# Performance work log

Measured on AMD Instinct MI355X. Metric: run time of the kernel, lower is better.

## Reference

```python
import jax, jax.numpy as jnp
import numpy as np

D_MODEL = 1024
HEADS = 16
SEQ = 2048
BATCH = 4
NEG_INF = -1e9
LN_EPS = 1e-5


def setup_inputs() -> dict:
    key = jax.random.key(0)
    ks = jax.random.split(key, 10)
    B, S, D = BATCH, SEQ, D_MODEL
    # xavier_uniform bound for square D x D linear
    bound = np.sqrt(6.0 / (D + D))
    def xavier(k):
        return jax.random.uniform(k, (D, D), jnp.float32, -bound, bound)
    return {
        "q": jax.random.normal(ks[0], (B, S, D), jnp.float32),
        "k": jax.random.normal(ks[1], (B, S, D), jnp.float32),
        "v": jax.random.normal(ks[2], (B, S, D), jnp.float32),
        "Wq": xavier(ks[3]),
        "Wk": xavier(ks[4]),
        "Wv": xavier(ks[5]),
        "Wo": xavier(ks[6]),
        "ln_gamma": jnp.ones((D,), jnp.float32),
        "ln_beta": jnp.zeros((D,), jnp.float32),
        "sen_len": jax.random.randint(ks[7], (B,), 1, S + 1, jnp.int32),
    }


def reference(q, k, v, Wq, Wk, Wv, Wo, ln_gamma, ln_beta, sen_len):
    B, S, D = q.shape
    H = HEADS
    d = D // H
    residual = q
    # projections (Linear with weight W applies x @ W.T)
    qh = jnp.einsum('bsd,ed->bse', q, Wq).reshape(B, S, H, d).transpose(0, 2, 1, 3)
    kh = jnp.einsum('bsd,ed->bse', k, Wk).reshape(B, S, H, d).transpose(0, 2, 1, 3)
    vh = jnp.einsum('bsd,ed->bse', v, Wv).reshape(B, S, H, d).transpose(0, 2, 1, 3)
    # scores [B,H,S,S]
    scores = jnp.einsum('bhqd,bhkd->bhqk', qh, kh) / np.sqrt(d).astype(np.float32)
    # padding mask on keys: j >= sen_len[b]; causal mask: j > i
    pad = jnp.arange(S)[None, :] >= sen_len[:, None]          # [B, S]
    causal = jnp.triu(jnp.ones((S, S), bool), 1)               # [S, S]
    mask = pad[:, None, None, :] | causal[None, None, :, :]
    scores = jnp.where(mask, NEG_INF, scores)
    att = jax.nn.softmax(scores, axis=-1)
    ctx = jnp.einsum('bhqk,bhkd->bhqd', att, vh)               # [B,H,S,d]
    ctx = ctx.transpose(0, 2, 1, 3).reshape(B, S, D)
    out = jnp.einsum('bsd,ed->bse', ctx, Wo)
    out = out + residual
    mean = out.mean(-1, keepdims=True)
    var = out.var(-1, keepdims=True)
    out = (out - mean) * jax.lax.rsqrt(var + LN_EPS) * ln_gamma + ln_beta
    return out
```

## Files before the change

### kernel.cpp

```cpp
#include <hip/hip_runtime.h>

typedef __bf16 bf16;
typedef bf16 bf16x8 __attribute__((ext_vector_type(8)));
typedef bf16 bf16x4 __attribute__((ext_vector_type(4)));
typedef float f32x4 __attribute__((ext_vector_type(4)));

#define ASYNC16(gp, lp) __builtin_amdgcn_global_load_lds( \
    (__attribute__((address_space(1))) void*)(const void*)(gp), \
    (__attribute__((address_space(3))) void*)(lp), 16, 0, 0)

__device__ __forceinline__ bf16x8 cvt2(const float4 a, const float4 b) {
    bf16x8 t;
    t[0] = (bf16)a.x; t[1] = (bf16)a.y; t[2] = (bf16)a.z; t[3] = (bf16)a.w;
    t[4] = (bf16)b.x; t[5] = (bf16)b.y; t[6] = (bf16)b.z; t[7] = (bf16)b.w;
    return t;
}

__global__ __launch_bounds__(256)
void cvt_w1(const float* __restrict__ W, bf16* __restrict__ out)
{
    const int i = blockIdx.x * 256 + threadIdx.x;
    const float4 a = ((const float4*)W)[i * 2];
    const float4 b = ((const float4*)W)[i * 2 + 1];
    *(bf16x8*)&out[(size_t)i * 8] = cvt2(a, b);
}

__global__ __launch_bounds__(256)
void cvt_w3(const float* __restrict__ W0, const float* __restrict__ W1,
            const float* __restrict__ W2, bf16* __restrict__ out)
{
    const int z = blockIdx.y;
    const float* src = (z == 0) ? W0 : (z == 1) ? W1 : W2;
    const int i = blockIdx.x * 256 + threadIdx.x;
    const float4 a = ((const float4*)src)[i * 2];
    const float4 b = ((const float4*)src)[i * 2 + 1];
    *(bf16x8*)&out[((size_t)z << 20) + (size_t)i * 8] = cvt2(a, b);
}

__global__ __launch_bounds__(256, 2)
void proj_gemm(const float* __restrict__ q, const float* __restrict__ k,
               const float* __restrict__ v, const bf16* __restrict__ Wb3,
               const int* __restrict__ sen_len,
               bf16* __restrict__ Qp, bf16* __restrict__ Kp, bf16* __restrict__ Vt)
{
    constexpr int K = 1024;
    __shared__ __align__(16) bf16 As[2][128 * 32];
    __shared__ __align__(16) bf16 Bs[2][128 * 32];

    const int z = blockIdx.z;
    const int flat = blockIdx.y * 8 + blockIdx.x;
    const int m0   = (flat & 63) * 128;
    const int n0   = (flat >> 6) * 128;

    if (z != 0) {
        const int s0 = m0 & 2047;
        if (s0 >= sen_len[m0 >> 11]) return;
    }

    const float* A = (z == 0) ? q : (z == 1) ? k : v;
    const bf16* W = Wb3 + ((size_t)z << 20);

    const int tid  = threadIdx.x;
    const int lane = tid & 63;
    const int w    = tid >> 6;
    const int wr   = w >> 1, wc = w & 1;

    f32x4 acc[4][4] = {};

    for (int k0 = 0; k0 < K; k0 += 64) {
        #pragma unroll
        for (int half = 0; half < 2; ++half) {
            #pragma unroll
            for (int i = 0; i < 2; ++i) {
                const int c   = w * 128 + i * 64 + lane;
                const int row = c >> 2, kg = c & 3;
                const int kb  = k0 + half * 32 + kg * 8;
                ASYNC16(W + (size_t)(n0 + row) * K + kb, &Bs[half][c * 8]);
                const float* ap = A + (size_t)(m0 + row) * K + kb;
                *(bf16x8*)&As[half][c * 8] = cvt2(*(const float4*)ap, *(const float4*)(ap + 4));
            }
        }
        __syncthreads();
        #pragma unroll
        for (int kk = 0; kk < 2; ++kk) {
            bf16x8 af[4], bfr[4];
            #pragma unroll
            for (int t = 0; t < 4; ++t) {
                af[t]  = *(const bf16x8*)&As[kk][(wr * 64 + t * 16 + (lane & 15)) * 32 + (lane >> 4) * 8];
                bfr[t] = *(const bf16x8*)&Bs[kk][(wc * 64 + t * 16 + (lane & 15)) * 32 + (lane >> 4) * 8];
            }
            #pragma unroll
            for (int mt = 0; mt < 4; ++mt)
                #pragma unroll
                for (int nt = 0; nt < 4; ++nt)
                    acc[mt][nt] = __builtin_amdgcn_mfma_f32_16x16x32_bf16(af[mt], bfr[nt], acc[mt][nt], 0, 0, 0);
        }
        __syncthreads();
    }

    #pragma unroll
    for (int mt = 0; mt < 4; ++mt) {
        #pragma unroll
        for (int nt = 0; nt < 4; ++nt) {
            const int mbase = m0 + wr * 64 + mt * 16 + ((lane >> 4) << 2);
            const int n     = n0 + wc * 64 + nt * 16 + (lane & 15);
            if (z < 2) {
                bf16* out = (z == 0) ? Qp : Kp;
                #pragma unroll
                for (int r = 0; r < 4; ++r)
                    out[(size_t)(mbase + r) * 1024 + n] = (bf16)acc[mt][nt][r];
            } else {
                const int h = n >> 6, dd = n & 63;
                const int b = mbase >> 11, s = mbase & 2047;
                bf16x4 v4;
                #pragma unroll
                for (int r = 0; r < 4; ++r) v4[r] = (bf16)acc[mt][nt][r];
                *(bf16x4*)&Vt[(((size_t)(b * 16 + h)) * 64 + dd) * 2048 + s] = v4;
            }
        }
    }
}

__global__ __launch_bounds__(256, 2)
void gemm_out(const bf16* __restrict__ A, const bf16* __restrict__ W,
              const float* __restrict__ R, float* __restrict__ out)
{
    constexpr int K = 1024;
    __shared__ __align__(16) bf16 As[2][128 * 32];
    __shared__ __align__(16) bf16 Bs[2][128 * 32];

    const int tid  = threadIdx.x;
    const int lane = tid & 63;
    const int w    = tid >> 6;
    const int wr   = w >> 1, wc = w & 1;
    const int flat = blockIdx.y * 8 + blockIdx.x;
    const int m0   = (flat & 63) * 128;
    const int n0   = (flat >> 6) * 128;

    f32x4 acc[4][4] = {};

    for (int k0 = 0; k0 < K; k0 += 64) {
        #pragma unroll
        for (int half = 0; half < 2; ++half) {
            #pragma unroll
            for (int i = 0; i < 2; ++i) {
                const int c   = w * 128 + i * 64 + lane;
                const int row = c >> 2, kg = c & 3;
                const int kb  = k0 + half * 32 + kg * 8;
                ASYNC16(A + (size_t)(m0 + row) * K + kb, &As[half][c * 8]);
                ASYNC16(W + (size_t)(n0 + row) * K + kb, &Bs[half][c * 8]);
            }
        }
        __syncthreads();
        #pragma unroll
        for (int kk = 0; kk < 2; ++kk) {
            bf16x8 af[4], bfr[4];
            #pragma unroll
            for (int t = 0; t < 4; ++t) {
                af[t]  = *(const bf16x8*)&As[kk][(wr * 64 + t * 16 + (lane & 15)) * 32 + (lane >> 4) * 8];
                bfr[t] = *(const bf16x8*)&Bs[kk][(wc * 64 + t * 16 + (lane & 15)) * 32 + (lane >> 4) * 8];
            }
            #pragma unroll
            for (int mt = 0; mt < 4; ++mt)
                #pragma unroll
                for (int nt = 0; nt < 4; ++nt)
                    acc[mt][nt] = __builtin_amdgcn_mfma_f32_16x16x32_bf16(af[mt], bfr[nt], acc[mt][nt], 0, 0, 0);
        }
        __syncthreads();
    }

    #pragma unroll
    for (int mt = 0; mt < 4; ++mt) {
        #pragma unroll
        for (int nt = 0; nt < 4; ++nt) {
            const int mbase = m0 + wr * 64 + mt * 16 + ((lane >> 4) << 2);
            const int n     = n0 + wc * 64 + nt * 16 + (lane & 15);
            #pragma unroll
            for (int r = 0; r < 4; ++r) {
                const size_t idx = (size_t)(mbase + r) * 1024 + n;
                out[idx] = acc[mt][nt][r] + R[idx];
            }
        }
    }
}

__global__ __launch_bounds__(256, 2)
void attn_kernel(const bf16* __restrict__ Qp, const bf16* __restrict__ Kp,
                 const bf16* __restrict__ Vt, const int* __restrict__ sen_len,
                 bf16* __restrict__ ctx)
{
    const int qt = gridDim.x - 1 - blockIdx.x;
    const int h = blockIdx.y, b = blockIdx.z;
    const int q0 = qt * 128;
    const int slen = sen_len[b];
    const int tid = threadIdx.x, lane = tid & 63, w = tid >> 6;
    const int wr = w >> 1, wc = w & 1;
    const float SCALE = 0.125f;
    const float SHIFT = 20.0f;

    __shared__ __align__(16) bf16 Ps[128 * 136];
    __shared__ float psum[2][128];

    bf16x8 qf[4][2];
    const bf16* Qbase = Qp + ((size_t)(b * 2048 + q0)) * 1024 + h * 64;
    #pragma unroll
    for (int mt = 0; mt < 4; ++mt)
        #pragma unroll
        for (int kk = 0; kk < 2; ++kk)
            qf[mt][kk] = *(const bf16x8*)(Qbase + (size_t)(wr * 64 + mt * 16 + (lane & 15)) * 1024
                                          + kk * 32 + (lane >> 4) * 8);

    f32x4 o[4][2] = {};
    float lsum[4][4] = {};

    const int jlim = min(q0 + 128, slen);
    const int nkt  = (jlim + 127) >> 7;

    const bf16* Kbh = Kp + (size_t)b * 2048 * 1024 + h * 64;
    const bf16* Vbh = Vt + (size_t)(b * 16 + h) * 64 * 2048;

    for (int kt = 0; kt < nkt; ++kt) {
        const int k0 = kt * 128;

        f32x4 sf[4][4] = {};
        #pragma unroll
        for (int kk = 0; kk < 2; ++kk) {
            bf16x8 bk[4];
            #pragma unroll
            for (int nt = 0; nt < 4; ++nt)
                bk[nt] = *(const bf16x8*)(Kbh + (size_t)(k0 + wc * 64 + nt * 16 + (lane & 15)) * 1024
                                          + kk * 32 + (lane >> 4) * 8);
            #pragma unroll
            for (int mt = 0; mt < 4; ++mt)
                #pragma unroll
                for (int nt = 0; nt < 4; ++nt)
                    sf[mt][nt] = __builtin_amdgcn_mfma_f32_16x16x32_bf16(qf[mt][kk], bk[nt], sf[mt][nt], 0, 0, 0);
        }

        if (kt == nkt - 1) {
            #pragma unroll
            for (int mt = 0; mt < 4; ++mt)
                #pragma unroll
                for (int r = 0; r < 4; ++r) {
                    const int row = wr * 64 + mt * 16 + ((lane >> 4) << 2) + r;
                    const int ig = q0 + row;
                    #pragma unroll
                    for (int nt = 0; nt < 4; ++nt) {
                        const int jg = k0 + wc * 64 + nt * 16 + (lane & 15);
                        const float sv = (jg > ig || jg >= slen) ? -1.0e9f : sf[mt][nt][r];
                        const float p = __expf(fmaf(sv, SCALE, -SHIFT));
                        lsum[mt][r] += p;
                        Ps[row * 136 + wc * 64 + nt * 16 + (lane & 15)] = (bf16)p;
                    }
                }
        } else {
            #pragma unroll
            for (int mt = 0; mt < 4; ++mt)
                #pragma unroll
                for (int r = 0; r < 4; ++r) {
                    const int row = wr * 64 + mt * 16 + ((lane >> 4) << 2) + r;
                    #pragma unroll
                    for (int nt = 0; nt < 4; ++nt) {
                        const float p = __expf(fmaf(sf[mt][nt][r], SCALE, -SHIFT));
                        lsum[mt][r] += p;
                        Ps[row * 136 + wc * 64 + nt * 16 + (lane & 15)] = (bf16)p;
                    }
                }
        }
        __syncthreads();

        #pragma unroll
        for (int ks = 0; ks < 4; ++ks) {
            bf16x8 pf[4], vf[2];
            #pragma unroll
            for (int mt = 0; mt < 4; ++mt)
                pf[mt] = *(const bf16x8*)&Ps[(wr * 64 + mt * 16 + (lane & 15)) * 136
                                             + ks * 32 + (lane >> 4) * 8];
            #pragma unroll
            for (int nt = 0; nt < 2; ++nt)
                vf[nt] = *(const bf16x8*)(Vbh + (size_t)(wc * 32 + nt * 16 + (lane & 15)) * 2048
                                          + k0 + ks * 32 + (lane >> 4) * 8);
            #pragma unroll
            for (int mt = 0; mt < 4; ++mt)
                #pragma unroll
                for (int nt = 0; nt < 2; ++nt)
                    o[mt][nt] = __builtin_amdgcn_mfma_f32_16x16x32_bf16(pf[mt], vf[nt], o[mt][nt], 0, 0, 0);
        }
        __syncthreads();
    }

    #pragma unroll
    for (int off = 1; off < 16; off <<= 1)
        #pragma unroll
        for (int mt = 0; mt < 4; ++mt)
            #pragma unroll
            for (int r = 0; r < 4; ++r)
                lsum[mt][r] += __shfl_xor(lsum[mt][r], off, 64);
    if ((lane & 15) == 0)
        #pragma unroll
        for (int mt = 0; mt < 4; ++mt)
            #pragma unroll
            for (int r = 0; r < 4; ++r)
                psum[wc][wr * 64 + mt * 16 + ((lane >> 4) << 2) + r] = lsum[mt][r];
    __syncthreads();

    #pragma unroll
    for (int mt = 0; mt < 4; ++mt)
        #pragma unroll
        for (int r = 0; r < 4; ++r) {
            const int row = wr * 64 + mt * 16 + ((lane >> 4) << 2) + r;
            const float inv = 1.0f / (psum[0][row] + psum[1][row]);
            const int sg = q0 + row;
            #pragma unroll
            for (int nt = 0; nt < 2; ++nt) {
                const int dd = wc * 32 + nt * 16 + (lane & 15);
                ctx[((size_t)(b * 2048 + sg)) * 1024 + h * 64 + dd] = (bf16)(o[mt][nt][r] * inv);
            }
        }
}

__global__ __launch_bounds__(256)
void ln_kernel(const float* __restrict__ y, const float* __restrict__ gamma,
               const float* __restrict__ beta, float* __restrict__ out)
{
    const int row = blockIdx.x;
    const int tid = threadIdx.x;
    const float4 v = ((const float4*)(y + (size_t)row * 1024))[tid];
    float s  = v.x + v.y + v.z + v.w;
    float s2 = v.x * v.x + v.y * v.y + v.z * v.z + v.w * v.w;
    #pragma unroll
    for (int o = 32; o > 0; o >>= 1) {
        s  += __shfl_down(s, o, 64);
        s2 += __shfl_down(s2, o, 64);
    }
    __shared__ float ps[4], ps2[4], stat[2];
    const int w = tid >> 6, lane = tid & 63;
    if (lane == 0) { ps[w] = s; ps2[w] = s2; }
    __syncthreads();
    if (tid == 0) {
        const float S  = ps[0] + ps[1] + ps[2] + ps[3];
        const float S2 = ps2[0] + ps2[1] + ps2[2] + ps2[3];
        const float mean = S * (1.0f / 1024.0f);
        const float var  = S2 * (1.0f / 1024.0f) - mean * mean;
        stat[0] = mean;
        stat[1] = rsqrtf(var + 1e-5f);
    }
    __syncthreads();
    const float mean = stat[0], rstd = stat[1];
    const float4 g4 = ((const float4*)gamma)[tid];
    const float4 b4 = ((const float4*)beta)[tid];
    float4 ov;
    ov.x = (v.x - mean) * rstd * g4.x + b4.x;
    ov.y = (v.y - mean) * rstd * g4.y + b4.y;
    ov.z = (v.z - mean) * rstd * g4.z + b4.z;
    ov.w = (v.w - mean) * rstd * g4.w + b4.w;
    ((float4*)(out + (size_t)row * 1024))[tid] = ov;
}

extern "C" void kernel_launch(void* const* d_in, const int* in_sizes, int n_in,
                              void* d_out, int out_size, void* d_ws, size_t ws_size,
                              hipStream_t stream)
{
    const float* q     = (const float*)d_in[0];
    const float* k     = (const float*)d_in[1];
    const float* v     = (const float*)d_in[2];
    const float* Wq    = (const float*)d_in[3];
    const float* Wk    = (const float*)d_in[4];
    const float* Wv    = (const float*)d_in[5];
    const float* Wo    = (const float*)d_in[6];
    const float* gamma = (const float*)d_in[7];
    const float* beta  = (const float*)d_in[8];
    const int*   sen   = (const int*)d_in[9];

    char* ws = (char*)d_ws;
    const size_t SEG = 16777216;
    bf16* Qp  = (bf16*)(ws);
    bf16* Kp  = (bf16*)(ws + SEG);
    bf16* Vt  = (bf16*)(ws + 2 * SEG);
    bf16* Wb3 = (bf16*)(ws + 3 * SEG);
    bf16* WoB = (bf16*)(ws + 3 * SEG);
    float* y  = (float*)ws;
    bf16* ctx = (bf16*)d_out;

    dim3 bb(256);
    cvt_w3<<<dim3(512, 3), bb, 0, stream>>>(Wq, Wk, Wv, Wb3);
    proj_gemm<<<dim3(8, 64, 3), bb, 0, stream>>>(q, k, v, Wb3, sen, Qp, Kp, Vt);
    attn_kernel<<<dim3(16, 16, 4), bb, 0, stream>>>(Qp, Kp, Vt, sen, ctx);
    cvt_w1<<<dim3(512), bb, 0, stream>>>(Wo, WoB);
    gemm_out<<<dim3(8, 64), bb, 0, stream>>>(ctx, WoB, q, y);
    ln_kernel<<<dim3(8192), bb, 0, stream>>>(y, gamma, beta, (float*)d_out);
}
```

Baseline: 310.2 us.

## Double-buffer projection and output GEMMs to overlap loads with MFMA

Rewrites the K loops of proj_gemm and gemm_out as a software pipeline. The next 32-wide K slice is prefetched into the other shared buffer while MFMAs run on the current one, and each step ends with a single barrier. In proj_gemm the fp32 A loads are issued early into registers and converted and stored after compute. The A tile is padded to a row stride of 40 to reduce LDS bank conflicts. The aim is to hide global memory latency behind compute, at the cost of more register pressure and twice as many barrier iterations. There is also a possible race: global_load_lds writes into the next buffer may not be complete at the barrier without an explicit vmcnt wait.

```diff
diff --git a/kernel.cpp b/kernel.cpp
--- a/kernel.cpp
+++ b/kernel.cpp
@@ -43,8 +43,10 @@
                const int* __restrict__ sen_len,
                bf16* __restrict__ Qp, bf16* __restrict__ Kp, bf16* __restrict__ Vt)
 {
-    constexpr int K = 1024;
-    __shared__ __align__(16) bf16 As[2][128 * 32];
+    constexpr int K  = 1024;
+    constexpr int NT = K / 32;
+    constexpr int AP = 40;
+    __shared__ __align__(16) bf16 As[2][128 * AP];
     __shared__ __align__(16) bf16 Bs[2][128 * 32];
 
     const int z = blockIdx.z;
@@ -65,35 +67,51 @@
     const int w    = tid >> 6;
     const int wr   = w >> 1, wc = w & 1;
 
+    const int c0 = tid,       r0 = c0 >> 2, g0 = c0 & 3;
+    const int c1 = tid + 256, r1 = c1 >> 2, g1 = c1 & 3;
+
     f32x4 acc[4][4] = {};
 
-    for (int k0 = 0; k0 < K; k0 += 64) {
-        #pragma unroll
-        for (int half = 0; half < 2; ++half) {
-            #pragma unroll
-            for (int i = 0; i < 2; ++i) {
-                const int c   = w * 128 + i * 64 + lane;
-                const int row = c >> 2, kg = c & 3;
-                const int kb  = k0 + half * 32 + kg * 8;
-                ASYNC16(W + (size_t)(n0 + row) * K + kb, &Bs[half][c * 8]);
-                const float* ap = A + (size_t)(m0 + row) * K + kb;
-                *(bf16x8*)&As[half][c * 8] = cvt2(*(const float4*)ap, *(const float4*)(ap + 4));
-            }
-        }
-        __syncthreads();
-        #pragma unroll
-        for (int kk = 0; kk < 2; ++kk) {
-            bf16x8 af[4], bfr[4];
-            #pragma unroll
-            for (int t = 0; t < 4; ++t) {
-                af[t]  = *(const bf16x8*)&As[kk][(wr * 64 + t * 16 + (lane & 15)) * 32 + (lane >> 4) * 8];
-                bfr[t] = *(const bf16x8*)&Bs[kk][(wc * 64 + t * 16 + (lane & 15)) * 32 + (lane >> 4) * 8];
-            }
-            #pragma unroll
-            for (int mt = 0; mt < 4; ++mt)
-                #pragma unroll
-                for (int nt = 0; nt < 4; ++nt)
-                    acc[mt][nt] = __builtin_amdgcn_mfma_f32_16x16x32_bf16(af[mt], bfr[nt], acc[mt][nt], 0, 0, 0);
+    {
+        const float* ap0 = A + (size_t)(m0 + r0) * K + g0 * 8;
+        const float* ap1 = A + (size_t)(m0 + r1) * K + g1 * 8;
+        const float4 a0 = *(const float4*)ap0, a1 = *(const float4*)(ap0 + 4);
+        const float4 a2 = *(const float4*)ap1, a3 = *(const float4*)(ap1 + 4);
+        ASYNC16(W + (size_t)(n0 + r0) * K + g0 * 8, &Bs[0][c0 * 8]);
+        ASYNC16(W + (size_t)(n0 + r1) * K + g1 * 8, &Bs[0][c1 * 8]);
+        *(bf16x8*)&As[0][r0 * AP + g0 * 8] = cvt2(a0, a1);
+        *(bf16x8*)&As[0][r1 * AP + g1 * 8] = cvt2(a2, a3);
+    }
+    __syncthreads();
+
+    #pragma unroll 2
+    for (int t = 0; t < NT; ++t) {
+        const int cur = t & 1, nxt = cur ^ 1;
+        float4 av0, av1, av2, av3;
+        const bool more = (t + 1 < NT);
+        if (more) {
+            const int kb = (t + 1) * 32;
+            const float* ap0 = A + (size_t)(m0 + r0) * K + kb + g0 * 8;
+            const float* ap1 = A + (size_t)(m0 + r1) * K + kb + g1 * 8;
+            av0 = *(const float4*)ap0; av1 = *(const float4*)(ap0 + 4);
+            av2 = *(const float4*)ap1; av3 = *(const float4*)(ap1 + 4);
+            ASYNC16(W + (size_t)(n0 + r0) * K + kb + g0 * 8, &Bs[nxt][c0 * 8]);
+            ASYNC16(W + (size_t)(n0 + r1) * K + kb + g1 * 8, &Bs[nxt][c1 * 8]);
+        }
+        bf16x8 af[4], bfr[4];
+        #pragma unroll
+        for (int tt = 0; tt < 4; ++tt) {
+            af[tt]  = *(const bf16x8*)&As[cur][(wr * 64 + tt * 16 + (lane & 15)) * AP + (lane >> 4) * 8];
+            bfr[tt] = *(const bf16x8*)&Bs[cur][(wc * 64 + tt * 16 + (lane & 15)) * 32 + (lane >> 4) * 8];
+        }
+        #pragma unroll
+        for (int mt = 0; mt < 4; ++mt)
+            #pragma unroll
+            for (int nt = 0; nt < 4; ++nt)
+                acc[mt][nt] = __builtin_amdgcn_mfma_f32_16x16x32_bf16(af[mt], bfr[nt], acc[mt][nt], 0, 0, 0);
+        if (more) {
+            *(bf16x8*)&As[nxt][r0 * AP + g0 * 8] = cvt2(av0, av1);
+            *(bf16x8*)&As[nxt][r1 * AP + g1 * 8] = cvt2(av2, av3);
         }
         __syncthreads();
     }
@@ -125,7 +143,8 @@
 void gemm_out(const bf16* __restrict__ A, const bf16* __restrict__ W,
               const float* __restrict__ R, float* __restrict__ out)
 {
-    constexpr int K = 1024;
+    constexpr int K  = 1024;
+    constexpr int NT = K / 32;
     __shared__ __align__(16) bf16 As[2][128 * 32];
     __shared__ __align__(16) bf16 Bs[2][128 * 32];
 
@@ -137,35 +156,40 @@
     const int m0   = (flat & 63) * 128;
     const int n0   = (flat >> 6) * 128;
 
+    const int c0 = tid,       r0 = c0 >> 2, g0 = c0 & 3;
+    const int c1 = tid + 256, r1 = c1 >> 2, g1 = c1 & 3;
+
     f32x4 acc[4][4] = {};
 
-    for (int k0 = 0; k0 < K; k0 += 64) {
-        #pragma unroll
-        for (int half = 0; half < 2; ++half) {
-            #pragma unroll
-            for (int i = 0; i < 2; ++i) {
-                const int c   = w * 128 + i * 64 + lane;
-                const int row = c >> 2, kg = c & 3;
-                const int kb  = k0 + half * 32 + kg * 8;
-                ASYNC16(A + (size_t)(m0 + row) * K + kb, &As[half][c * 8]);
-                ASYNC16(W + (size_t)(n0 + row) * K + kb, &Bs[half][c * 8]);
-            }
-        }
-        __syncthreads();
-        #pragma unroll
-        for (int kk = 0; kk < 2; ++kk) {
-            bf16x8 af[4], bfr[4];
-            #pragma unroll
-            for (int t = 0; t < 4; ++t) {
-                af[t]  = *(const bf16x8*)&As[kk][(wr * 64 + t * 16 + (lane & 15)) * 32 + (lane >> 4) * 8];
-                bfr[t] = *(const bf16x8*)&Bs[kk][(wc * 64 + t * 16 + (lane & 15)) * 32 + (lane >> 4) * 8];
-            }
-            #pragma unroll
-            for (int mt = 0; mt < 4; ++mt)
-                #pragma unroll
-                for (int nt = 0; nt < 4; ++nt)
-                    acc[mt][nt] = __builtin_amdgcn_mfma_f32_16x16x32_bf16(af[mt], bfr[nt], acc[mt][nt], 0, 0, 0);
-        }
+    {
+        ASYNC16(A + (size_t)(m0 + r0) * K + g0 * 8, &As[0][c0 * 8]);
+        ASYNC16(A + (size_t)(m0 + r1) * K + g1 * 8, &As[0][c1 * 8]);
+        ASYNC16(W + (size_t)(n0 + r0) * K + g0 * 8, &Bs[0][c0 * 8]);
+        ASYNC16(W + (size_t)(n0 + r1) * K + g1 * 8, &Bs[0][c1 * 8]);
+    }
+    __syncthreads();
+
+    #pragma unroll 2
+    for (int t = 0; t < NT; ++t) {
+        const int cur = t & 1, nxt = cur ^ 1;
+        if (t + 1 < NT) {
+            const int kb = (t + 1) * 32;
+            ASYNC16(A + (size_t)(m0 + r0) * K + kb + g0 * 8, &As[nxt][c0 * 8]);
+            ASYNC16(A + (size_t)(m0 + r1) * K + kb + g1 * 8, &As[nxt][c1 * 8]);
+            ASYNC16(W + (size_t)(n0 + r0) * K + kb + g0 * 8, &Bs[nxt][c0 * 8]);
+            ASYNC16(W + (size_t)(n0 + r1) * K + kb + g1 * 8, &Bs[nxt][c1 * 8]);
+        }
+        bf16x8 af[4], bfr[4];
+        #pragma unroll
+        for (int tt = 0; tt < 4; ++tt) {
+            af[tt]  = *(const bf16x8*)&As[cur][(wr * 64 + tt * 16 + (lane & 15)) * 32 + (lane >> 4) * 8];
+            bfr[tt] = *(const bf16x8*)&Bs[cur][(wc * 64 + tt * 16 + (lane & 15)) * 32 + (lane >> 4) * 8];
+        }
+        #pragma unroll
+        for (int mt = 0; mt < 4; ++mt)
+            #pragma unroll
+            for (int nt = 0; nt < 4; ++nt)
+                acc[mt][nt] = __builtin_amdgcn_mfma_f32_16x16x32_bf16(af[mt], bfr[nt], acc[mt][nt], 0, 0, 0);
         __syncthreads();
     }
 
```

Result: slower. 341.0 us (+9.9%).

## Software-pipeline projection and output GEMMs with 4-stage LDS ring and prefetch

Applied to the files above, without the earlier changes.

The projection and output GEMM main loops move from a load-then-sync-then-compute loop with two barriers per K step to a 4-slot LDS ring. Loads for tile k+2 are issued while tile k is computed, and manual vmcnt waits plus a single barrier per phase keep slots in order. In the projection GEMM, fp32 activations are prefetched into registers and converted to bf16 one phase later. This hides global memory latency behind MFMA work, at the cost of more shared memory (64KB per block, which may limit occupancy to 2 blocks) and fragile hand-written waitcnt ordering.

```diff
diff --git a/kernel.cpp b/kernel.cpp
--- a/kernel.cpp
+++ b/kernel.cpp
@@ -8,6 +8,10 @@
 #define ASYNC16(gp, lp) __builtin_amdgcn_global_load_lds( \
     (__attribute__((address_space(1))) void*)(const void*)(gp), \
     (__attribute__((address_space(3))) void*)(lp), 16, 0, 0)
+
+#define S_VMCNT(N) asm volatile("s_waitcnt vmcnt(" #N ")" ::: "memory")
+#define S_LGKM0    asm volatile("s_waitcnt lgkmcnt(0)" ::: "memory")
+#define S_BAR      __builtin_amdgcn_s_barrier()
 
 __device__ __forceinline__ bf16x8 cvt2(const float4 a, const float4 b) {
     bf16x8 t;
@@ -43,9 +47,10 @@
                const int* __restrict__ sen_len,
                bf16* __restrict__ Qp, bf16* __restrict__ Kp, bf16* __restrict__ Vt)
 {
-    constexpr int K = 1024;
-    __shared__ __align__(16) bf16 As[2][128 * 32];
-    __shared__ __align__(16) bf16 Bs[2][128 * 32];
+    constexpr int K  = 1024;
+    constexpr int NT = 32;
+    __shared__ __align__(16) bf16 Asr[4][128 * 32];
+    __shared__ __align__(16) bf16 Bsr[4][128 * 32];
 
     const int z = blockIdx.z;
     const int flat = blockIdx.y * 8 + blockIdx.x;
@@ -65,38 +70,67 @@
     const int w    = tid >> 6;
     const int wr   = w >> 1, wc = w & 1;
 
+    const int c0 = tid,       r0 = c0 >> 2, g0 = c0 & 3;
+    const int c1 = tid + 256, r1 = c1 >> 2, g1 = c1 & 3;
+    const float* Ab0 = A + (size_t)(m0 + r0) * K + g0 * 8;
+    const float* Ab1 = A + (size_t)(m0 + r1) * K + g1 * 8;
+    const bf16*  Wb0 = W + (size_t)(n0 + r0) * K + g0 * 8;
+    const bf16*  Wb1 = W + (size_t)(n0 + r1) * K + g1 * 8;
+
+    float4 rA[2][4];
     f32x4 acc[4][4] = {};
 
-    for (int k0 = 0; k0 < K; k0 += 64) {
-        #pragma unroll
-        for (int half = 0; half < 2; ++half) {
-            #pragma unroll
-            for (int i = 0; i < 2; ++i) {
-                const int c   = w * 128 + i * 64 + lane;
-                const int row = c >> 2, kg = c & 3;
-                const int kb  = k0 + half * 32 + kg * 8;
-                ASYNC16(W + (size_t)(n0 + row) * K + kb, &Bs[half][c * 8]);
-                const float* ap = A + (size_t)(m0 + row) * K + kb;
-                *(bf16x8*)&As[half][c * 8] = cvt2(*(const float4*)ap, *(const float4*)(ap + 4));
-            }
-        }
-        __syncthreads();
-        #pragma unroll
-        for (int kk = 0; kk < 2; ++kk) {
-            bf16x8 af[4], bfr[4];
-            #pragma unroll
-            for (int t = 0; t < 4; ++t) {
-                af[t]  = *(const bf16x8*)&As[kk][(wr * 64 + t * 16 + (lane & 15)) * 32 + (lane >> 4) * 8];
-                bfr[t] = *(const bf16x8*)&Bs[kk][(wc * 64 + t * 16 + (lane & 15)) * 32 + (lane >> 4) * 8];
-            }
-            #pragma unroll
-            for (int mt = 0; mt < 4; ++mt)
-                #pragma unroll
-                for (int nt = 0; nt < 4; ++nt)
-                    acc[mt][nt] = __builtin_amdgcn_mfma_f32_16x16x32_bf16(af[mt], bfr[nt], acc[mt][nt], 0, 0, 0);
-        }
-        __syncthreads();
-    }
+#define P_ISSUE_A(ph, RI) do { \
+        rA[RI][0] = *(const float4*)(Ab0 + (ph) * 32); \
+        rA[RI][1] = *(const float4*)(Ab0 + (ph) * 32 + 4); \
+        rA[RI][2] = *(const float4*)(Ab1 + (ph) * 32); \
+        rA[RI][3] = *(const float4*)(Ab1 + (ph) * 32 + 4); } while (0)
+#define P_ISSUE_B(ph, PI) do { \
+        ASYNC16(Wb0 + (ph) * 32, &Bsr[PI][c0 * 8]); \
+        ASYNC16(Wb1 + (ph) * 32, &Bsr[PI][c1 * 8]); } while (0)
+#define P_WRITE_A(PW, RW) do { \
+        *(bf16x8*)&Asr[PW][c0 * 8] = cvt2(rA[RW][0], rA[RW][1]); \
+        *(bf16x8*)&Asr[PW][c1 * 8] = cvt2(rA[RW][2], rA[RW][3]); } while (0)
+#define P_COMPUTE(PC) do { \
+        bf16x8 af[4], bfr[4]; \
+        _Pragma("unroll") \
+        for (int t = 0; t < 4; ++t) { \
+            af[t]  = *(const bf16x8*)&Asr[PC][(wr * 64 + t * 16 + (lane & 15)) * 32 + (lane >> 4) * 8]; \
+            bfr[t] = *(const bf16x8*)&Bsr[PC][(wc * 64 + t * 16 + (lane & 15)) * 32 + (lane >> 4) * 8]; \
+        } \
+        _Pragma("unroll") \
+        for (int mt = 0; mt < 4; ++mt) \
+            _Pragma("unroll") \
+            for (int nt = 0; nt < 4; ++nt) \
+                acc[mt][nt] = __builtin_amdgcn_mfma_f32_16x16x32_bf16(af[mt], bfr[nt], acc[mt][nt], 0, 0, 0); \
+    } while (0)
+
+#define P_PHASE(h, PC, PI, PW, RW, RI) do { \
+        P_COMPUTE(PC); \
+        if ((h) + 2 < NT) { P_ISSUE_A((h) + 2, RI); P_ISSUE_B((h) + 2, PI); } \
+        if ((h) + 1 < NT) { \
+            if ((h) + 2 < NT) { S_VMCNT(6); } else { S_VMCNT(0); } \
+            P_WRITE_A(PW, RW); \
+            S_LGKM0; S_BAR; \
+        } } while (0)
+
+    P_ISSUE_A(0, 0); P_ISSUE_B(0, 0);
+    P_ISSUE_A(1, 1); P_ISSUE_B(1, 1);
+    S_VMCNT(6);
+    P_WRITE_A(0, 0);
+    S_LGKM0; S_BAR;
+
+    for (int hb = 0; hb < NT; hb += 4) {
+        P_PHASE(hb + 0, 0, 2, 1, 1, 0);
+        P_PHASE(hb + 1, 1, 3, 2, 0, 1);
+        P_PHASE(hb + 2, 2, 0, 3, 1, 0);
+        P_PHASE(hb + 3, 3, 1, 0, 0, 1);
+    }
+#undef P_PHASE
+#undef P_COMPUTE
+#undef P_WRITE_A
+#undef P_ISSUE_B
+#undef P_ISSUE_A
 
     #pragma unroll
     for (int mt = 0; mt < 4; ++mt) {
@@ -125,9 +159,10 @@
 void gemm_out(const bf16* __restrict__ A, const bf16* __restrict__ W,
               const float* __restrict__ R, float* __restrict__ out)
 {
-    constexpr int K = 1024;
-    __shared__ __align__(16) bf16 As[2][128 * 32];
-    __shared__ __align__(16) bf16 Bs[2][128 * 32];
+    constexpr int K  = 1024;
+    constexpr int NT = 32;
+    __shared__ __align__(16) bf16 Asr[4][128 * 32];
+    __shared__ __align__(16) bf16 Bsr[4][128 * 32];
 
     const int tid  = threadIdx.x;
     const int lane = tid & 63;
@@ -137,37 +172,55 @@
     const int m0   = (flat & 63) * 128;
     const int n0   = (flat >> 6) * 128;
 
+    const int c0 = tid,       r0 = c0 >> 2, g0 = c0 & 3;
+    const int c1 = tid + 256, r1 = c1 >> 2, g1 = c1 & 3;
+    const bf16* Ab0 = A + (size_t)(m0 + r0) * K + g0 * 8;
+    const bf16* Ab1 = A + (size_t)(m0 + r1) * K + g1 * 8;
+    const bf16* Wb0 = W + (size_t)(n0 + r0) * K + g0 * 8;
+    const bf16* Wb1 = W + (size_t)(n0 + r1) * K + g1 * 8;
+
     f32x4 acc[4][4] = {};
 
-    for (int k0 = 0; k0 < K; k0 += 64) {
-        #pragma unroll
-        for (int half = 0; half < 2; ++half) {
-            #pragma unroll
-            for (int i = 0; i < 2; ++i) {
-                const int c   = w * 128 + i * 64 + lane;
-                const int row = c >> 2, kg = c & 3;
-                const int kb  = k0 + half * 32 + kg * 8;
-                ASYNC16(A + (size_t)(m0 + row) * K + kb, &As[half][c * 8]);
-                ASYNC16(W + (size_t)(n0 + row) * K + kb, &Bs[half][c * 8]);
-            }
-        }
-        __syncthreads();
-        #pragma unroll
-        for (int kk = 0; kk < 2; ++kk) {
-            bf16x8 af[4], bfr[4];
-            #pragma unroll
-            for (int t = 0; t < 4; ++t) {
-                af[t]  = *(const bf16x8*)&As[kk][(wr * 64 + t * 16 + (lane & 15)) * 32 + (lane >> 4) * 8];
-                bfr[t] = *(const bf16x8*)&Bs[kk][(wc * 64 + t * 16 + (lane & 15)) * 32 + (lane >> 4) * 8];
-            }
-            #pragma unroll
-            for (int mt = 0; mt < 4; ++mt)
-                #pragma unroll
-                for (int nt = 0; nt < 4; ++nt)
-                    acc[mt][nt] = __builtin_amdgcn_mfma_f32_16x16x32_bf16(af[mt], bfr[nt], acc[mt][nt], 0, 0, 0);
-        }
-        __syncthreads();
-    }
+#define G_ISSUE(ph, PI) do { \
+        ASYNC16(Ab0 + (ph) * 32, &Asr[PI][c0 * 8]); \
+        ASYNC16(Ab1 + (ph) * 32, &Asr[PI][c1 * 8]); \
+        ASYNC16(Wb0 + (ph) * 32, &Bsr[PI][c0 * 8]); \
+        ASYNC16(Wb1 + (ph) * 32, &Bsr[PI][c1 * 8]); } while (0)
+#define G_COMPUTE(PC) do { \
+        bf16x8 af[4], bfr[4]; \
+        _Pragma("unroll") \
+        for (int t = 0; t < 4; ++t) { \
+            af[t]  = *(const bf16x8*)&Asr[PC][(wr * 64 + t * 16 + (lane & 15)) * 32 + (lane >> 4) * 8]; \
+            bfr[t] = *(const bf16x8*)&Bsr[PC][(wc * 64 + t * 16 + (lane & 15)) * 32 + (lane >> 4) * 8]; \
+        } \
+        _Pragma("unroll") \
+        for (int mt = 0; mt < 4; ++mt) \
+            _Pragma("unroll") \
+            for (int nt = 0; nt < 4; ++nt) \
+                acc[mt][nt] = __builtin_amdgcn_mfma_f32_16x16x32_bf16(af[mt], bfr[nt], acc[mt][nt], 0, 0, 0); \
+    } while (0)
+#define G_PHASE(h, PC, PI) do { \
+        G_COMPUTE(PC); \
+        if ((h) + 2 < NT) { G_ISSUE((h) + 2, PI); } \
+        if ((h) + 1 < NT) { \
+            if ((h) + 2 < NT) { S_VMCNT(4); } else { S_VMCNT(0); } \
+            S_BAR; \
+        } } while (0)
+
+    G_ISSUE(0, 0);
+    G_ISSUE(1, 1);
+    S_VMCNT(4);
+    S_BAR;
+
+    for (int hb = 0; hb < NT; hb += 4) {
+        G_PHASE(hb + 0, 0, 2);
+        G_PHASE(hb + 1, 1, 3);
+        G_PHASE(hb + 2, 2, 0);
+        G_PHASE(hb + 3, 3, 1);
+    }
+#undef G_PHASE
+#undef G_COMPUTE
+#undef G_ISSUE
 
     #pragma unroll
     for (int mt = 0; mt < 4; ++mt) {
```

After: 331.0 us. 1.07x slower.
